# Kernel optimization log

Hardware: AMD Instinct MI355X
Metric: run time of the kernel (lower is better)

Reference implementation:

```python
import jax, jax.numpy as jnp
import numpy as np

KSIZE = 3   # patch kernel
NSIZE = 7   # search neighborhood
SCALE = 4   # downscale factor
ALPHA = 1


def _patches(x, k, pad_mode):
    # x: [b,c,h,w] -> [b, c*k*k, h, w], feature ordering channel-major
    # (matches torch.nn.functional.unfold ordering).
    if pad_mode == 'reflect':
        p = k // 2
        xp = jnp.pad(x, ((0, 0), (0, 0), (p, p), (p, p)), mode='reflect')
        return jax.lax.conv_general_dilated_patches(xp, (k, k), (1, 1), 'VALID')
    return jax.lax.conv_general_dilated_patches(x, (k, k), (1, 1), 'SAME')


def census(x):
    # UFlow-style soft census transform (the CensusTransform used in this repo):
    # grayscale*255, 3x3 zero-padded patches minus center, soft-sign normalize.
    gray = (0.299 * x[:, 0:1] + 0.587 * x[:, 1:2] + 0.114 * x[:, 2:3]) * 255.0
    p = _patches(gray, KSIZE, 'zero')          # [b, 9, h, w]
    t = p - gray
    return t / jnp.sqrt(0.81 + t * t)


def downsample(x):
    b, c, h, w = x.shape
    return jax.image.resize(x, (b, c, h // SCALE, w // SCALE), method='cubic')


def unfold_center(x):
    # _unfold(data, with_unfold=False): [b,c,h,w] -> [b, hw, c*k*k]
    x = downsample(x)
    b, c, h, w = x.shape
    p = _patches(x, KSIZE, 'reflect').reshape(b, c * KSIZE * KSIZE, h * w)
    return p.transpose(0, 2, 1)


def unfold_nbr(x):
    # _unfold(data, with_unfold=True): [b,c,h,w] -> [b, hw, n*n, c*k*k]
    x = downsample(x)
    b, c, h, w = x.shape
    d1 = _patches(x, KSIZE, 'reflect')          # [b, c*k*k, h, w]
    c1 = d1.shape[1]
    d2 = _patches(d1, NSIZE, 'reflect')         # [b, c1*n*n, h, w]
    d2 = d2.reshape(b, c1, NSIZE * NSIZE, h * w)
    return d2.transpose(0, 3, 2, 1)


def reference(pred, I):
    # --- census-space distance + argmin over 2*n*n candidates ---
    p_ct = unfold_center(census(pred))                       # [b, hw, 81]
    nbr_ct = jnp.concatenate(
        [unfold_nbr(census(I[:, 0])), unfold_nbr(census(I[:, 1]))], axis=2
    )                                                        # [b, hw, 2n^2, 81]
    # ||p - n||^2 expanded as p2 + n2 - 2 p.n (avoids the huge repeated diff)
    p2 = jnp.sum(p_ct * p_ct, axis=-1)                       # [b, hw]
    n2 = jnp.sum(nbr_ct * nbr_ct, axis=-1)                   # [b, hw, 2n^2]
    dis = p2[:, :, None] + n2 - 2.0 * jnp.einsum('bpc,bpnc->bpn', p_ct, nbr_ct)
    ind = jnp.argmin(dis, axis=2)                            # [b, hw]
    # --- gather matched raw patches and compute loss ---
    p = unfold_center(pred)                                  # [b, hw, 27]
    nbr = jnp.concatenate(
        [unfold_nbr(I[:, 0]), unfold_nbr(I[:, 1])], axis=2
    )                                                        # [b, hw, 2n^2, 27]
    matched = jnp.take_along_axis(nbr, ind[:, :, None, None], axis=2)[:, :, 0]
    return jnp.mean((p - matched) ** 2 * 0.5)


def setup_inputs() -> dict:
    key = jax.random.key(0)
    k1, k2 = jax.random.split(key)
    pred = jax.random.normal(k1, (2, 3, 384, 384), dtype=jnp.float32)
    I = jax.random.normal(k2, (2, 2, 3, 384, 384), dtype=jnp.float32)
    return {'pred': pred, 'I': I}
```

## Files before the change

kernel.cpp:

```cpp
#include <hip/hip_runtime.h>
#include <math.h>

#define FH 384
#define FW 384
#define DH 96
#define DW 96
#define NIMG 6
#define PLANE (DH * DW)
#define NPIX (2 * PLANE)

__device__ __forceinline__ float keysc(float x) {
    if (x < 1.f) return ((1.5f * x - 2.5f) * x) * x + 1.f;
    if (x < 2.f) return ((-0.5f * x + 2.5f) * x - 4.f) * x + 2.f;
    return 0.f;
}

__device__ __forceinline__ int refl(int i, int n) {
    if (i < 0) i = -i;
    if (i >= n) i = 2 * (n - 1) - i;
    return i;
}

__device__ __forceinline__ int clampi(int i) { return min(max(i, 0), 95); }

__device__ __forceinline__ float softsign(float t) {
    return t / sqrtf(0.81f + t * t);
}

__global__ void k_gray(const float* __restrict__ pred, const float* __restrict__ I,
                       float* __restrict__ gray) {
    int idx = blockIdx.x * 256 + threadIdx.x;
    const int total = NIMG * FH * FW;
    if (idx >= total) return;
    int img = idx / (FH * FW);
    int px  = idx % (FH * FW);
    const float* src;
    if (img < 2) {
        src = pred + img * 3 * FH * FW;
    } else {
        int j = (img - 2) >> 1, b = (img - 2) & 1;
        src = I + ((b * 2 + j) * 3) * FH * FW;
    }
    float r = src[px], g = src[FH * FW + px], b = src[2 * FH * FW + px];
    gray[idx] = (0.299f * r + 0.587f * g + 0.114f * b) * 255.0f;
}

__global__ __launch_bounds__(256) void k_census_downH(const float* __restrict__ gray,
                                                      float* __restrict__ CH) {
    int idx = blockIdx.x * 256 + threadIdx.x;
    const int total = NIMG * DH * FW;
    if (idx >= total) return;
    int x   = idx % FW;
    int t1  = idx / FW;
    int yo  = t1 % DH;
    int img = t1 / DH;
    const float* g = gray + img * FH * FW;

    bool xl = (x > 0), xr = (x < FW - 1);

    float a0, a1, a2, b0, b1, b2, c0, c1, c2;
    auto loadrow = [&](int r, float& v0, float& v1, float& v2) {
        if (r < 0 || r >= FH) { v0 = v1 = v2 = 0.f; return; }
        const float* gr = g + r * FW + x;
        v1 = gr[0];
        v0 = xl ? gr[-1] : 0.f;
        v2 = xr ? gr[1] : 0.f;
    };

    int rbase = 4 * yo - 6;
    loadrow(rbase - 1, a0, a1, a2);
    loadrow(rbase,     b0, b1, b2);

    float acc0 = 0.f, acc1 = 0.f, acc2 = 0.f, acc3 = 0.f, acc5 = 0.f,
          acc6 = 0.f, acc7 = 0.f, acc8 = 0.f, z = 0.f;
#pragma unroll
    for (int t = 0; t < 16; ++t) {
        int r = rbase + t;
        loadrow(r + 1, c0, c1, c2);
        if (r >= 0 && r < FH) {
            float w = keysc(fabsf((float)t - 7.5f) * 0.25f);
            z += w;
            float gc = b1;
            acc0 += w * softsign(a0 - gc);
            acc1 += w * softsign(a1 - gc);
            acc2 += w * softsign(a2 - gc);
            acc3 += w * softsign(b0 - gc);
            acc5 += w * softsign(b2 - gc);
            acc6 += w * softsign(c0 - gc);
            acc7 += w * softsign(c1 - gc);
            acc8 += w * softsign(c2 - gc);
        }
        a0 = b0; a1 = b1; a2 = b2;
        b0 = c0; b1 = c1; b2 = c2;
    }
    float inv = 1.f / z;
    float* o = CH + (img * 9 * DH + yo) * FW + x;
    const int STR = DH * FW;
    o[0 * STR] = acc0 * inv;
    o[1 * STR] = acc1 * inv;
    o[2 * STR] = acc2 * inv;
    o[3 * STR] = acc3 * inv;
    o[4 * STR] = 0.f;
    o[5 * STR] = acc5 * inv;
    o[6 * STR] = acc6 * inv;
    o[7 * STR] = acc7 * inv;
    o[8 * STR] = acc8 * inv;
}

__global__ void k_downW(const float* __restrict__ src, float* __restrict__ dst, int nrows) {
    int idx = blockIdx.x * 256 + threadIdx.x;
    int total = nrows * DW;
    if (idx >= total) return;
    int xo = idx % DW;
    int row = idx / DW;
    const float* s = src + row * FW;
    float acc = 0.f, z = 0.f;
#pragma unroll
    for (int t = 0; t < 16; ++t) {
        int i = 4 * xo - 6 + t;
        if (i < 0 || i >= FW) continue;
        float w = keysc(fabsf((float)t - 7.5f) * 0.25f);
        z += w;
        acc += w * s[i];
    }
    dst[idx] = acc / z;
}

__global__ void k_raw_downH(const float* __restrict__ pred, const float* __restrict__ I,
                            float* __restrict__ RH) {
    int idx = blockIdx.x * 256 + threadIdx.x;
    const int total = NIMG * 3 * DH * FW;
    if (idx >= total) return;
    int x  = idx % FW;
    int t1 = idx / FW;
    int yo = t1 % DH;
    int t2 = t1 / DH;
    int c  = t2 % 3;
    int img = t2 / 3;
    const float* src;
    if (img < 2) {
        src = pred + (img * 3 + c) * FH * FW;
    } else {
        int j = (img - 2) >> 1, b = (img - 2) & 1;
        src = I + (((b * 2 + j) * 3) + c) * FH * FW;
    }
    float acc = 0.f, z = 0.f;
#pragma unroll
    for (int t = 0; t < 16; ++t) {
        int r = 4 * yo - 6 + t;
        if (r < 0 || r >= FH) continue;
        float w = keysc(fabsf((float)t - 7.5f) * 0.25f);
        z += w;
        acc += w * src[r * FW + x];
    }
    RH[idx] = acc / z;
}

__global__ void k_n2(const float* __restrict__ CD, float* __restrict__ N2) {
    int idx = blockIdx.x * 256 + threadIdx.x;
    if (idx >= 4 * PLANE) return;
    int img4 = idx / PLANE;
    int pos  = idx % PLANE;
    int y = pos / DW, x = pos % DW;
    int ry[3], rx[3];
#pragma unroll
    for (int kk = 0; kk < 3; ++kk) {
        ry[kk] = refl(y + kk - 1, DH);
        rx[kk] = refl(x + kk - 1, DW);
    }
    const float* C = CD + (2 + img4) * 9 * PLANE;
    float s = 0.f;
#pragma unroll
    for (int c = 0; c < 9; ++c)
#pragma unroll
        for (int ky = 0; ky < 3; ++ky)
#pragma unroll
            for (int kx = 0; kx < 3; ++kx) {
                float v = C[c * PLANE + ry[ky] * DW + rx[kx]];
                s += v * v;
            }
    N2[idx] = s;
}

__global__ __launch_bounds__(256, 1) void k_match(const float* __restrict__ CD,
                                                  const float* __restrict__ N2,
                                                  const float* __restrict__ RD,
                                                  float* __restrict__ partial) {
    __shared__ float nb[2][9][9][40];
    __shared__ float ct[9][3][34];
    __shared__ float sbd[256];
    __shared__ int   sbn[256];
    __shared__ float red[32];

    int bid = blockIdx.x;
    int b   = bid / 288;
    int rem = bid % 288;
    int y   = rem / 3;
    int x0  = (rem % 3) * 32;

    int px = threadIdx.x & 31;
    int g  = threadIdx.x >> 5;
    int x  = x0 + px;

    for (int idx = threadIdx.x; idx < 2 * 9 * 9 * 40; idx += 256) {
        int j   = idx / 3240;
        int r1  = idx % 3240;
        int c   = r1 / 360;
        int r2  = r1 % 360;
        int u   = r2 / 40;
        int v   = r2 % 40;
        int gy  = clampi(y - 4 + u);
        int gx  = clampi(x0 - 4 + v);
        nb[j][c][u][v] = CD[((2 + 2 * j + b) * 9 + c) * PLANE + gy * DW + gx];
    }
    for (int idx = threadIdx.x; idx < 9 * 3 * 34; idx += 256) {
        int c = idx / 102;
        int r1 = idx % 102;
        int u = r1 / 34;
        int v = r1 % 34;
        int gy = clampi(y - 1 + u);
        int gx = clampi(x0 - 1 + v);
        ct[c][u][v] = CD[(b * 9 + c) * PLANE + gy * DW + gx];
    }
    __syncthreads();

    int cy_s[3], cx_s[3];
#pragma unroll
    for (int kk = 0; kk < 3; ++kk) {
        cy_s[kk] = refl(y + kk - 1, DH) - (y - 1);
        cx_s[kk] = refl(x + kk - 1, DW) - (x0 - 1);
    }
    float p[81];
#pragma unroll
    for (int c = 0; c < 9; ++c)
#pragma unroll
        for (int ky = 0; ky < 3; ++ky)
#pragma unroll
            for (int kx = 0; kx < 3; ++kx)
                p[c * 9 + ky * 3 + kx] = ct[c][cy_s[ky]][cx_s[kx]];

    float best = INFINITY;
    int bn = 1 << 30;
    for (int k = 0; k < 13; ++k) {
        int n = 8 * k + g;
        if (n >= 98) break;
        int j = n / 49, rr = n % 49;
        int dy = rr / 7 - 3, dx = rr % 7 - 3;
        int yy = refl(y + dy, DH), xx = refl(x + dx, DW);
        int ry_s[3], rx_s[3];
#pragma unroll
        for (int kk = 0; kk < 3; ++kk) {
            ry_s[kk] = refl(yy + kk - 1, DH) - (y - 4);
            rx_s[kk] = refl(xx + kk - 1, DW) - (x0 - 4);
        }
        float dot = 0.f;
#pragma unroll
        for (int c = 0; c < 9; ++c)
#pragma unroll
            for (int ky = 0; ky < 3; ++ky)
#pragma unroll
                for (int kx = 0; kx < 3; ++kx)
                    dot += p[c * 9 + ky * 3 + kx] * nb[j][c][ry_s[ky]][rx_s[kx]];
        float dis = N2[(2 * j + b) * PLANE + yy * DW + xx] - 2.f * dot;
        if (dis < best) { best = dis; bn = n; }
    }
    sbd[threadIdx.x] = best;
    sbn[threadIdx.x] = bn;
    __syncthreads();

    if (g == 0) {
        float d0 = sbd[px];
        int   n0 = sbn[px];
#pragma unroll
        for (int gg = 1; gg < 8; ++gg) {
            float d = sbd[gg * 32 + px];
            int   n = sbn[gg * 32 + px];
            if (d < d0 || (d == d0 && n < n0)) { d0 = d; n0 = n; }
        }
        int j = n0 / 49, rr = n0 % 49;
        int dy = rr / 7 - 3, dx = rr % 7 - 3;
        int yy = refl(y + dy, DH), xx = refl(x + dx, DW);
        int ry0[3], rx0[3], ry[3], rx[3];
#pragma unroll
        for (int kk = 0; kk < 3; ++kk) {
            ry0[kk] = refl(y + kk - 1, DH);
            rx0[kk] = refl(x + kk - 1, DW);
            ry[kk]  = refl(yy + kk - 1, DH);
            rx[kk]  = refl(xx + kk - 1, DW);
        }
        const float* RDp = RD + b * 3 * PLANE;
        const float* RDn = RD + (2 + 2 * j + b) * 3 * PLANE;
        float loss = 0.f;
#pragma unroll
        for (int c = 0; c < 3; ++c)
#pragma unroll
            for (int ky = 0; ky < 3; ++ky)
#pragma unroll
                for (int kx = 0; kx < 3; ++kx) {
                    float a = RDp[c * PLANE + ry0[ky] * DW + rx0[kx]];
                    float m = RDn[c * PLANE + ry[ky] * DW + rx[kx]];
                    float d = a - m;
                    loss += d * d;
                }
        red[px] = loss;
    }
    __syncthreads();
    if (threadIdx.x == 0) {
        float s = 0.f;
#pragma unroll
        for (int i = 0; i < 32; ++i) s += red[i];
        partial[bid] = s;
    }
}

#define NPART 576
__global__ void k_final(const float* __restrict__ partial, float* __restrict__ out) {
    __shared__ float red[256];
    float v = 0.f;
    for (int i = threadIdx.x; i < NPART; i += 256) v += partial[i];
    red[threadIdx.x] = v;
    __syncthreads();
#pragma unroll
    for (int s = 128; s > 0; s >>= 1) {
        if (threadIdx.x < s) red[threadIdx.x] += red[threadIdx.x + s];
        __syncthreads();
    }
    if (threadIdx.x == 0) out[0] = red[0] * (0.5f / 497664.0f);
}

extern "C" void kernel_launch(void* const* d_in, const int* in_sizes, int n_in,
                              void* d_out, int out_size, void* d_ws, size_t ws_size,
                              hipStream_t stream) {
    const float* pred = (const float*)d_in[0];
    const float* I    = (const float*)d_in[1];
    float* out = (float*)d_out;
    float* ws  = (float*)d_ws;

    float* CD   = ws;
    float* RD   = CD + 497664;
    float* S    = RD + 165888;
    float* gray = S;
    float* CH   = S + 884736;
    float* RH   = CH + 1990656;
    float* N2   = S;
    float* part = S + 36864;

    k_gray<<<(NIMG * FH * FW + 255) / 256, 256, 0, stream>>>(pred, I, gray);
    k_census_downH<<<(NIMG * DH * FW + 255) / 256, 256, 0, stream>>>(gray, CH);
    k_raw_downH<<<(NIMG * 3 * DH * FW + 255) / 256, 256, 0, stream>>>(pred, I, RH);
    k_downW<<<((NIMG * 12 * DH) * DW + 255) / 256, 256, 0, stream>>>(CH, CD, NIMG * 12 * DH);
    k_n2<<<(4 * PLANE + 255) / 256, 256, 0, stream>>>(CD, N2);
    k_match<<<576, 256, 0, stream>>>(CD, N2, RD, part);
    k_final<<<1, 256, 0, stream>>>(part, out);
}
```

Baseline: 134.7 us.

## Fuse census downsample into one kernel and split match by frame with combine pass

Merges the grayscale, census-vertical-downsample and horizontal-downsample steps into one kernel that keeps intermediates in shared memory, removing two large global round trips. The match kernel is split across the two reference frames, doubling the block count and halving its shared-memory tile. A new combine kernel picks the better of the two per-pixel minima and computes the loss. The cost is an extra launch plus a small global buffer of per-pixel best distances and indices.

```diff
diff --git a/kernel.cpp b/kernel.cpp
--- a/kernel.cpp
+++ b/kernel.cpp
@@ -27,13 +27,17 @@
     return t / sqrtf(0.81f + t * t);
 }
 
-__global__ void k_gray(const float* __restrict__ pred, const float* __restrict__ I,
-                       float* __restrict__ gray) {
-    int idx = blockIdx.x * 256 + threadIdx.x;
-    const int total = NIMG * FH * FW;
-    if (idx >= total) return;
-    int img = idx / (FH * FW);
-    int px  = idx % (FH * FW);
+__global__ __launch_bounds__(384) void k_census_down(const float* __restrict__ pred,
+                                                     const float* __restrict__ I,
+                                                     float* __restrict__ CD) {
+    __shared__ float g[18][FW];
+    __shared__ float ct[9][FW];
+
+    int bid = blockIdx.x;
+    int img = bid / DH;
+    int yo  = bid % DH;
+    int tid = threadIdx.x;
+
     const float* src;
     if (img < 2) {
         src = pred + img * 3 * FH * FW;
@@ -41,70 +45,75 @@
         int j = (img - 2) >> 1, b = (img - 2) & 1;
         src = I + ((b * 2 + j) * 3) * FH * FW;
     }
-    float r = src[px], g = src[FH * FW + px], b = src[2 * FH * FW + px];
-    gray[idx] = (0.299f * r + 0.587f * g + 0.114f * b) * 255.0f;
-}
-
-__global__ __launch_bounds__(256) void k_census_downH(const float* __restrict__ gray,
-                                                      float* __restrict__ CH) {
-    int idx = blockIdx.x * 256 + threadIdx.x;
-    const int total = NIMG * DH * FW;
-    if (idx >= total) return;
-    int x   = idx % FW;
-    int t1  = idx / FW;
-    int yo  = t1 % DH;
-    int img = t1 / DH;
-    const float* g = gray + img * FH * FW;
-
-    bool xl = (x > 0), xr = (x < FW - 1);
-
-    float a0, a1, a2, b0, b1, b2, c0, c1, c2;
-    auto loadrow = [&](int r, float& v0, float& v1, float& v2) {
-        if (r < 0 || r >= FH) { v0 = v1 = v2 = 0.f; return; }
-        const float* gr = g + r * FW + x;
-        v1 = gr[0];
-        v0 = xl ? gr[-1] : 0.f;
-        v2 = xr ? gr[1] : 0.f;
-    };
 
     int rbase = 4 * yo - 6;
-    loadrow(rbase - 1, a0, a1, a2);
-    loadrow(rbase,     b0, b1, b2);
-
-    float acc0 = 0.f, acc1 = 0.f, acc2 = 0.f, acc3 = 0.f, acc5 = 0.f,
-          acc6 = 0.f, acc7 = 0.f, acc8 = 0.f, z = 0.f;
-#pragma unroll
-    for (int t = 0; t < 16; ++t) {
-        int r = rbase + t;
-        loadrow(r + 1, c0, c1, c2);
+    for (int u = 0; u < 18; ++u) {
+        int r = rbase - 1 + u;
+        float v = 0.f;
         if (r >= 0 && r < FH) {
+            const float* s = src + r * FW + tid;
+            v = (0.299f * s[0] + 0.587f * s[FH * FW] + 0.114f * s[2 * FH * FW]) * 255.0f;
+        }
+        g[u][tid] = v;
+    }
+    __syncthreads();
+
+    {
+        bool xl = (tid > 0), xr = (tid < FW - 1);
+        float a0, a1, a2, b0, b1, b2, c0, c1, c2;
+        a1 = g[0][tid]; a0 = xl ? g[0][tid - 1] : 0.f; a2 = xr ? g[0][tid + 1] : 0.f;
+        b1 = g[1][tid]; b0 = xl ? g[1][tid - 1] : 0.f; b2 = xr ? g[1][tid + 1] : 0.f;
+
+        float acc0 = 0.f, acc1 = 0.f, acc2 = 0.f, acc3 = 0.f, acc5 = 0.f,
+              acc6 = 0.f, acc7 = 0.f, acc8 = 0.f, z = 0.f;
+#pragma unroll
+        for (int t = 0; t < 16; ++t) {
+            int u = t + 2;
+            c1 = g[u][tid]; c0 = xl ? g[u][tid - 1] : 0.f; c2 = xr ? g[u][tid + 1] : 0.f;
+            int r = rbase + t;
+            if (r >= 0 && r < FH) {
+                float w = keysc(fabsf((float)t - 7.5f) * 0.25f);
+                z += w;
+                float gc = b1;
+                acc0 += w * softsign(a0 - gc);
+                acc1 += w * softsign(a1 - gc);
+                acc2 += w * softsign(a2 - gc);
+                acc3 += w * softsign(b0 - gc);
+                acc5 += w * softsign(b2 - gc);
+                acc6 += w * softsign(c0 - gc);
+                acc7 += w * softsign(c1 - gc);
+                acc8 += w * softsign(c2 - gc);
+            }
+            a0 = b0; a1 = b1; a2 = b2;
+            b0 = c0; b1 = c1; b2 = c2;
+        }
+        float inv = 1.f / z;
+        ct[0][tid] = acc0 * inv;
+        ct[1][tid] = acc1 * inv;
+        ct[2][tid] = acc2 * inv;
+        ct[3][tid] = acc3 * inv;
+        ct[4][tid] = 0.f;
+        ct[5][tid] = acc5 * inv;
+        ct[6][tid] = acc6 * inv;
+        ct[7][tid] = acc7 * inv;
+        ct[8][tid] = acc8 * inv;
+    }
+    __syncthreads();
+
+    for (int idx = tid; idx < 9 * DW; idx += 384) {
+        int ch = idx / DW;
+        int xo = idx % DW;
+        float acc = 0.f, z = 0.f;
+#pragma unroll
+        for (int t = 0; t < 16; ++t) {
+            int i = 4 * xo - 6 + t;
+            if (i < 0 || i >= FW) continue;
             float w = keysc(fabsf((float)t - 7.5f) * 0.25f);
             z += w;
-            float gc = b1;
-            acc0 += w * softsign(a0 - gc);
-            acc1 += w * softsign(a1 - gc);
-            acc2 += w * softsign(a2 - gc);
-            acc3 += w * softsign(b0 - gc);
-            acc5 += w * softsign(b2 - gc);
-            acc6 += w * softsign(c0 - gc);
-            acc7 += w * softsign(c1 - gc);
-            acc8 += w * softsign(c2 - gc);
-        }
-        a0 = b0; a1 = b1; a2 = b2;
-        b0 = c0; b1 = c1; b2 = c2;
-    }
-    float inv = 1.f / z;
-    float* o = CH + (img * 9 * DH + yo) * FW + x;
-    const int STR = DH * FW;
-    o[0 * STR] = acc0 * inv;
-    o[1 * STR] = acc1 * inv;
-    o[2 * STR] = acc2 * inv;
-    o[3 * STR] = acc3 * inv;
-    o[4 * STR] = 0.f;
-    o[5 * STR] = acc5 * inv;
-    o[6 * STR] = acc6 * inv;
-    o[7 * STR] = acc7 * inv;
-    o[8 * STR] = acc8 * inv;
+            acc += w * ct[ch][i];
+        }
+        CD[(img * 9 + ch) * PLANE + yo * DW + xo] = acc / z;
+    }
 }
 
 __global__ void k_downW(const float* __restrict__ src, float* __restrict__ dst, int nrows) {
@@ -184,17 +193,18 @@
 
 __global__ __launch_bounds__(256, 1) void k_match(const float* __restrict__ CD,
                                                   const float* __restrict__ N2,
-                                                  const float* __restrict__ RD,
-                                                  float* __restrict__ partial) {
-    __shared__ float nb[2][9][9][40];
+                                                  float* __restrict__ bestd,
+                                                  int* __restrict__ bestn) {
+    __shared__ float nb[9][9][40];
     __shared__ float ct[9][3][34];
     __shared__ float sbd[256];
     __shared__ int   sbn[256];
-    __shared__ float red[32];
 
     int bid = blockIdx.x;
-    int b   = bid / 288;
-    int rem = bid % 288;
+    int j   = bid / 576;
+    int sub = bid % 576;
+    int b   = sub / 288;
+    int rem = sub % 288;
     int y   = rem / 3;
     int x0  = (rem % 3) * 32;
 
@@ -202,22 +212,20 @@
     int g  = threadIdx.x >> 5;
     int x  = x0 + px;
 
-    for (int idx = threadIdx.x; idx < 2 * 9 * 9 * 40; idx += 256) {
-        int j   = idx / 3240;
-        int r1  = idx % 3240;
-        int c   = r1 / 360;
-        int r2  = r1 % 360;
-        int u   = r2 / 40;
-        int v   = r2 % 40;
-        int gy  = clampi(y - 4 + u);
-        int gx  = clampi(x0 - 4 + v);
-        nb[j][c][u][v] = CD[((2 + 2 * j + b) * 9 + c) * PLANE + gy * DW + gx];
+    for (int idx = threadIdx.x; idx < 9 * 9 * 40; idx += 256) {
+        int c  = idx / 360;
+        int r2 = idx % 360;
+        int u  = r2 / 40;
+        int v  = r2 % 40;
+        int gy = clampi(y - 4 + u);
+        int gx = clampi(x0 - 4 + v);
+        nb[c][u][v] = CD[((2 + 2 * j + b) * 9 + c) * PLANE + gy * DW + gx];
     }
     for (int idx = threadIdx.x; idx < 9 * 3 * 34; idx += 256) {
-        int c = idx / 102;
+        int c  = idx / 102;
         int r1 = idx % 102;
-        int u = r1 / 34;
-        int v = r1 % 34;
+        int u  = r1 / 34;
+        int v  = r1 % 34;
         int gy = clampi(y - 1 + u);
         int gx = clampi(x0 - 1 + v);
         ct[c][u][v] = CD[(b * 9 + c) * PLANE + gy * DW + gx];
@@ -238,31 +246,34 @@
 #pragma unroll
             for (int kx = 0; kx < 3; ++kx)
                 p[c * 9 + ky * 3 + kx] = ct[c][cy_s[ky]][cx_s[kx]];
+#pragma unroll
+    for (int f = 0; f < 81; ++f) asm volatile("" : "+v"(p[f]));
 
     float best = INFINITY;
     int bn = 1 << 30;
-    for (int k = 0; k < 13; ++k) {
-        int n = 8 * k + g;
-        if (n >= 98) break;
-        int j = n / 49, rr = n % 49;
-        int dy = rr / 7 - 3, dx = rr % 7 - 3;
-        int yy = refl(y + dy, DH), xx = refl(x + dx, DW);
-        int ry_s[3], rx_s[3];
-#pragma unroll
-        for (int kk = 0; kk < 3; ++kk) {
-            ry_s[kk] = refl(yy + kk - 1, DH) - (y - 4);
-            rx_s[kk] = refl(xx + kk - 1, DW) - (x0 - 4);
-        }
-        float dot = 0.f;
-#pragma unroll
-        for (int c = 0; c < 9; ++c)
-#pragma unroll
-            for (int ky = 0; ky < 3; ++ky)
-#pragma unroll
-                for (int kx = 0; kx < 3; ++kx)
-                    dot += p[c * 9 + ky * 3 + kx] * nb[j][c][ry_s[ky]][rx_s[kx]];
-        float dis = N2[(2 * j + b) * PLANE + yy * DW + xx] - 2.f * dot;
-        if (dis < best) { best = dis; bn = n; }
+#pragma unroll
+    for (int k = 0; k < 7; ++k) {
+        int rr = 8 * k + g;
+        if (rr < 49) {
+            int dy = rr / 7 - 3, dx = rr % 7 - 3;
+            int yy = refl(y + dy, DH), xx = refl(x + dx, DW);
+            int ry_s[3], rx_s[3];
+#pragma unroll
+            for (int kk = 0; kk < 3; ++kk) {
+                ry_s[kk] = refl(yy + kk - 1, DH) - (y - 4);
+                rx_s[kk] = refl(xx + kk - 1, DW) - (x0 - 4);
+            }
+            float dot = 0.f;
+#pragma unroll
+            for (int c = 0; c < 9; ++c)
+#pragma unroll
+                for (int ky = 0; ky < 3; ++ky)
+#pragma unroll
+                    for (int kx = 0; kx < 3; ++kx)
+                        dot += p[c * 9 + ky * 3 + kx] * nb[c][ry_s[ky]][rx_s[kx]];
+            float dis = N2[(2 * j + b) * PLANE + yy * DW + xx] - 2.f * dot;
+            if (dis < best) { best = dis; bn = j * 49 + rr; }
+        }
     }
     sbd[threadIdx.x] = best;
     sbn[threadIdx.x] = bn;
@@ -277,51 +288,72 @@
             int   n = sbn[gg * 32 + px];
             if (d < d0 || (d == d0 && n < n0)) { d0 = d; n0 = n; }
         }
-        int j = n0 / 49, rr = n0 % 49;
-        int dy = rr / 7 - 3, dx = rr % 7 - 3;
-        int yy = refl(y + dy, DH), xx = refl(x + dx, DW);
-        int ry0[3], rx0[3], ry[3], rx[3];
-#pragma unroll
-        for (int kk = 0; kk < 3; ++kk) {
-            ry0[kk] = refl(y + kk - 1, DH);
-            rx0[kk] = refl(x + kk - 1, DW);
-            ry[kk]  = refl(yy + kk - 1, DH);
-            rx[kk]  = refl(xx + kk - 1, DW);
-        }
-        const float* RDp = RD + b * 3 * PLANE;
-        const float* RDn = RD + (2 + 2 * j + b) * 3 * PLANE;
-        float loss = 0.f;
-#pragma unroll
-        for (int c = 0; c < 3; ++c)
-#pragma unroll
-            for (int ky = 0; ky < 3; ++ky)
-#pragma unroll
-                for (int kx = 0; kx < 3; ++kx) {
-                    float a = RDp[c * PLANE + ry0[ky] * DW + rx0[kx]];
-                    float m = RDn[c * PLANE + ry[ky] * DW + rx[kx]];
-                    float d = a - m;
-                    loss += d * d;
-                }
-        red[px] = loss;
-    }
-    __syncthreads();
-    if (threadIdx.x == 0) {
-        float s = 0.f;
-#pragma unroll
-        for (int i = 0; i < 32; ++i) s += red[i];
-        partial[bid] = s;
-    }
-}
-
-#define NPART 576
+        int pid = b * PLANE + y * DW + x;
+        bestd[j * NPIX + pid] = d0;
+        bestn[j * NPIX + pid] = n0;
+    }
+}
+
+__global__ __launch_bounds__(256) void k_combine(const float* __restrict__ bestd,
+                                                 const int* __restrict__ bestn,
+                                                 const float* __restrict__ RD,
+                                                 float* __restrict__ partial) {
+    int pid = blockIdx.x * 256 + threadIdx.x;
+    int b   = pid / PLANE;
+    int pos = pid % PLANE;
+    int y = pos / DW, x = pos % DW;
+
+    float d0 = bestd[pid];
+    int   n0 = bestn[pid];
+    float d1 = bestd[NPIX + pid];
+    int   n1 = bestn[NPIX + pid];
+    if (d1 < d0 || (d1 == d0 && n1 < n0)) { d0 = d1; n0 = n1; }
+
+    int j = n0 / 49, rr = n0 % 49;
+    int dy = rr / 7 - 3, dx = rr % 7 - 3;
+    int yy = refl(y + dy, DH), xx = refl(x + dx, DW);
+    int ry0[3], rx0[3], ry[3], rx[3];
+#pragma unroll
+    for (int kk = 0; kk < 3; ++kk) {
+        ry0[kk] = refl(y + kk - 1, DH);
+        rx0[kk] = refl(x + kk - 1, DW);
+        ry[kk]  = refl(yy + kk - 1, DH);
+        rx[kk]  = refl(xx + kk - 1, DW);
+    }
+    const float* RDp = RD + b * 3 * PLANE;
+    const float* RDn = RD + (2 + 2 * j + b) * 3 * PLANE;
+    float loss = 0.f;
+#pragma unroll
+    for (int c = 0; c < 3; ++c)
+#pragma unroll
+        for (int ky = 0; ky < 3; ++ky)
+#pragma unroll
+            for (int kx = 0; kx < 3; ++kx) {
+                float a = RDp[c * PLANE + ry0[ky] * DW + rx0[kx]];
+                float m = RDn[c * PLANE + ry[ky] * DW + rx[kx]];
+                float d = a - m;
+                loss += d * d;
+            }
+
+    __shared__ float red[256];
+    red[threadIdx.x] = loss;
+    __syncthreads();
+#pragma unroll
+    for (int s = 128; s > 0; s >>= 1) {
+        if (threadIdx.x < s) red[threadIdx.x] += red[threadIdx.x + s];
+        __syncthreads();
+    }
+    if (threadIdx.x == 0) partial[blockIdx.x] = red[0];
+}
+
+#define NPART 72
 __global__ void k_final(const float* __restrict__ partial, float* __restrict__ out) {
-    __shared__ float red[256];
-    float v = 0.f;
-    for (int i = threadIdx.x; i < NPART; i += 256) v += partial[i];
+    __shared__ float red[128];
+    float v = (threadIdx.x < NPART) ? partial[threadIdx.x] : 0.f;
     red[threadIdx.x] = v;
     __syncthreads();
 #pragma unroll
-    for (int s = 128; s > 0; s >>= 1) {
+    for (int s = 64; s > 0; s >>= 1) {
         if (threadIdx.x < s) red[threadIdx.x] += red[threadIdx.x + s];
         __syncthreads();
     }
@@ -339,17 +371,17 @@
     float* CD   = ws;
     float* RD   = CD + 497664;
     float* S    = RD + 165888;
-    float* gray = S;
-    float* CH   = S + 884736;
-    float* RH   = CH + 1990656;
+    float* RH   = S;
     float* N2   = S;
-    float* part = S + 36864;
-
-    k_gray<<<(NIMG * FH * FW + 255) / 256, 256, 0, stream>>>(pred, I, gray);
-    k_census_downH<<<(NIMG * DH * FW + 255) / 256, 256, 0, stream>>>(gray, CH);
+    float* bestd = S + 36864;
+    int*   bestn = (int*)(S + 73728);
+    float* part  = S + 110592;
+
+    k_census_down<<<NIMG * DH, 384, 0, stream>>>(pred, I, CD);
     k_raw_downH<<<(NIMG * 3 * DH * FW + 255) / 256, 256, 0, stream>>>(pred, I, RH);
-    k_downW<<<((NIMG * 12 * DH) * DW + 255) / 256, 256, 0, stream>>>(CH, CD, NIMG * 12 * DH);
+    k_downW<<<((NIMG * 3 * DH) * DW + 255) / 256, 256, 0, stream>>>(RH, RD, NIMG * 3 * DH);
     k_n2<<<(4 * PLANE + 255) / 256, 256, 0, stream>>>(CD, N2);
-    k_match<<<576, 256, 0, stream>>>(CD, N2, RD, part);
-    k_final<<<1, 256, 0, stream>>>(part, out);
-}
+    k_match<<<1152, 256, 0, stream>>>(CD, N2, bestd, bestn);
+    k_combine<<<NPIX / 256, 256, 0, stream>>>(bestd, bestn, RD, part);
+    k_final<<<1, 128, 0, stream>>>(part, out);
+}
```

New measurement: 138.6 us. +2.9%, slower.
